# Optimization experiments

Hardware: AMD Instinct MI355X
Metric: run time of the kernel (lower is better)

The kernel has to match this reference:

```python
import jax, jax.numpy as jnp
import numpy as np

N_OPS = 15  # Bell(4) equivariant basis for square 2nd-order -> 2nd-order

def setup_inputs() -> dict:
    key = jax.random.key(0)
    n = 100_000          # entity instances
    m = 1_000_000        # random off-diagonal pairs (mirrored -> symmetric pattern)
    d_in, d_out = 32, 32
    rng = np.random.default_rng(0)
    r = rng.integers(0, n, size=m)
    c = rng.integers(0, n, size=m)
    # symmetric sparsity pattern + full diagonal; nnz = 2m + n
    rows = np.concatenate([r, c, np.arange(n)]).astype(np.int32)
    cols = np.concatenate([c, r, np.arange(n)]).astype(np.int32)
    # transpose intersection: entry k <-> its mirrored entry
    trans_perm = np.concatenate([np.arange(m, 2 * m), np.arange(m),
                                 np.arange(2 * m, 2 * m + n)]).astype(np.int32)
    k1, k2 = jax.random.split(key)
    values = jax.random.normal(k1, (rows.shape[0], d_in), dtype=jnp.float32)
    stdv = 0.1 / np.sqrt(d_in)
    weights = jax.random.uniform(k2, (N_OPS, d_in, d_out), minval=-stdv, maxval=stdv,
                                 dtype=jnp.float32)
    bias = jnp.zeros((N_OPS,), jnp.float32)
    return {"values": values, "weights": weights, "bias": bias,
            "rows": jnp.asarray(rows), "cols": jnp.asarray(cols),
            "trans_perm": jnp.asarray(trans_perm), "n_nodes": n}


def reference(values, weights, bias, rows, cols, trans_perm, n_nodes):
    # values: [nnz, d_in] features of sparse matrix entries at (rows, cols)
    is_diag = (rows == cols)[:, None].astype(values.dtype)            # [nnz, 1]
    sum_r = jax.ops.segment_sum(values, rows, num_segments=n_nodes)   # pool over cols -> [n, d_in]
    sum_c = jax.ops.segment_sum(values, cols, num_segments=n_nodes)   # pool over rows -> [n, d_in]
    diag = jax.ops.segment_sum(values * is_diag, rows, num_segments=n_nodes)  # gather_diag -> [n, d_in]
    sum_all = values.sum(0)        # pool over both indices -> [d_in]
    diag_sum = diag.sum(0)         # pooled diagonal -> [d_in]
    W = weights
    # ops 1-2: identity intersection, transpose intersection
    out = values @ W[0] + values[trans_perm] @ W[1]
    # ops 3-8: pooled/diag vectors broadcast along rows or cols
    out += (sum_r @ W[2])[rows] + (sum_r @ W[3])[cols]
    out += (sum_c @ W[4])[rows] + (sum_c @ W[5])[cols]
    out += (diag @ W[6])[rows] + (diag @ W[7])[cols]
    # ops 9-12, 14: embedded into the diagonal of the output pattern
    diag_part = (sum_r @ W[8])[rows] + (sum_c @ W[9])[rows] + (diag @ W[10])[rows] \
                + (diag_sum @ W[11]) + (sum_all @ W[13])
    out += is_diag * diag_part
    # ops 13, 15: global scalars broadcast to every nnz
    out += diag_sum @ W[12] + sum_all @ W[14]
    # per-op scalar bias added to the whole output (Y = Y + op + bias[i])
    out += bias.sum()
    return out
```

## Files before the change

### kernel.cpp

```cpp
#include <hip/hip_runtime.h>

#define N_NODES 100000
#define D 32
#define CAP 40


__global__ void k1a_fill(const int* __restrict__ rows,
                         const int* __restrict__ cols,
                         const int* __restrict__ tp,
                         const float* __restrict__ values,
                         int nnz,
                         int* __restrict__ cnt,
                         int* __restrict__ list,
                         float* __restrict__ sum_r,
                         float* __restrict__ sum_c,
                         float* __restrict__ diag) {
  int e = blockIdx.x * blockDim.x + threadIdx.x;
  if (e >= nnz) return;
  int r = rows[e];
  int pos = atomicAdd(&cnt[r], 1);
  if (pos < CAP) {
    list[(size_t)r * CAP + pos] = e;
  } else {
    int t = tp[e];
    int c = cols[e];
    for (int f = 0; f < D; f++) {
      float ve = values[(size_t)e * D + f];
      unsafeAtomicAdd(&sum_r[(size_t)r * D + f], ve);
      unsafeAtomicAdd(&sum_c[(size_t)r * D + f], values[(size_t)t * D + f]);
      if (c == r) unsafeAtomicAdd(&diag[(size_t)r * D + f], ve);
    }
  }
}

__global__ void k1b_gather(const float* __restrict__ values,
                           const int* __restrict__ cols,
                           const int* __restrict__ tp,
                           const int* __restrict__ cnt,
                           const int* __restrict__ list,
                           int n,
                           float* __restrict__ sum_r,
                           float* __restrict__ sum_c,
                           float* __restrict__ diag) {
  int tid = blockIdx.x * blockDim.x + threadIdx.x;
  int f = tid & 31;
  int i = tid >> 5;
  if (i >= n) return;
  int m = cnt[i];
  if (m > CAP) m = CAP;
  const int* lst = list + (size_t)i * CAP;
  float accR = 0.f, accC = 0.f, accD = 0.f;
  int e = (m > 0) ? lst[0] : 0;
  for (int k = 0; k < m; k++) {
    int en = (k + 1 < m) ? lst[k + 1] : 0;
    int t = tp[e];
    int c = cols[e];
    float ve = values[(size_t)e * D + f];
    float vt = values[(size_t)t * D + f];
    accR += ve;
    accC += vt;
    if (c == i) accD += ve;
    e = en;
  }
  size_t o = (size_t)i * D + f;
  sum_r[o] += accR;
  sum_c[o] += accC;
  diag[o] += accD;
}

__global__ void k1c_reduce(const float* __restrict__ sum_r,
                           const float* __restrict__ diag,
                           int n,
                           float* __restrict__ sum_all,
                           float* __restrict__ diag_sum) {
  __shared__ float sa[D], sd[D];
  int tid = blockIdx.x * blockDim.x + threadIdx.x;
  int f = threadIdx.x & 31;
  int slot = tid >> 5;
  int nslots = (gridDim.x * blockDim.x) >> 5;
  if (threadIdx.x < D) { sa[threadIdx.x] = 0.f; sd[threadIdx.x] = 0.f; }
  __syncthreads();
  float la = 0.f, ld = 0.f;
  for (int i = slot; i < n; i += nslots) {
    la += sum_r[(size_t)i * D + f];
    ld += diag[(size_t)i * D + f];
  }
  atomicAdd(&sa[f], la);
  atomicAdd(&sd[f], ld);
  __syncthreads();
  if (threadIdx.x < D) {
    unsafeAtomicAdd(&sum_all[threadIdx.x], sa[threadIdx.x]);
    unsafeAtomicAdd(&diag_sum[threadIdx.x], sd[threadIdx.x]);
  }
}

__global__ void k1_segsums(const float* __restrict__ values,
                           const int* __restrict__ rows,
                           const int* __restrict__ cols,
                           int nnz,
                           float* __restrict__ sum_r,
                           float* __restrict__ sum_c,
                           float* __restrict__ diag,
                           float* __restrict__ sum_all,
                           float* __restrict__ diag_sum) {
  int tid = blockIdx.x * blockDim.x + threadIdx.x;
  int f = tid & 31;
  int slot = tid >> 5;
  int nslots = (gridDim.x * blockDim.x) >> 5;
  float local_all = 0.f, local_diag = 0.f;
  for (int e = slot; e < nnz; e += nslots) {
    float v = values[(size_t)e * D + f];
    int r = rows[e];
    int c = cols[e];
    unsafeAtomicAdd(&sum_r[(size_t)r * D + f], v);
    unsafeAtomicAdd(&sum_c[(size_t)c * D + f], v);
    local_all += v;
    if (r == c) {
      unsafeAtomicAdd(&diag[(size_t)r * D + f], v);
      local_diag += v;
    }
  }
  unsafeAtomicAdd(&sum_all[f], local_all);
  unsafeAtomicAdd(&diag_sum[f], local_diag);
}

__global__ void k_globals(const float* __restrict__ W,
                          const float* __restrict__ bias,
                          const float* __restrict__ sum_all,
                          const float* __restrict__ diag_sum,
                          float* __restrict__ g,
                          float* __restrict__ gd) {
  int j = threadIdx.x;
  if (j >= D) return;
  float bt = 0.f;
  for (int i = 0; i < 15; i++) bt += bias[i];
  float a = bt, b = 0.f;
  for (int k = 0; k < D; k++) {
    float ds = diag_sum[k];
    float sa = sum_all[k];
    a = fmaf(ds, W[12 * 1024 + k * D + j], a);
    a = fmaf(sa, W[14 * 1024 + k * D + j], a);
    b = fmaf(ds, W[11 * 1024 + k * D + j], b);
    b = fmaf(sa, W[13 * 1024 + k * D + j], b);
  }
  g[j] = a;
  gd[j] = b;
}

__device__ __forceinline__ void triple_acc(float accA[D], float accB[D], float accD[D],
                                           const float* __restrict__ src,
                                           const float* __restrict__ wa,
                                           const float* __restrict__ wb,
                                           const float* __restrict__ wd) {
  const float4* s4 = (const float4*)src;
  for (int q = 0; q < 8; q++) {
    float4 t = s4[q];
    const float* wa_q = wa + q * 128;
    const float* wb_q = wb + q * 128;
    const float* wd_q = wd + q * 128;
#pragma unroll
    for (int j = 0; j < D; j++) {
      float a = accA[j], b = accB[j], d = accD[j];
      a = fmaf(t.x, wa_q[j], a);
      a = fmaf(t.y, wa_q[32 + j], a);
      a = fmaf(t.z, wa_q[64 + j], a);
      a = fmaf(t.w, wa_q[96 + j], a);
      b = fmaf(t.x, wb_q[j], b);
      b = fmaf(t.y, wb_q[32 + j], b);
      b = fmaf(t.z, wb_q[64 + j], b);
      b = fmaf(t.w, wb_q[96 + j], b);
      d = fmaf(t.x, wd_q[j], d);
      d = fmaf(t.y, wd_q[32 + j], d);
      d = fmaf(t.z, wd_q[64 + j], d);
      d = fmaf(t.w, wd_q[96 + j], d);
      accA[j] = a; accB[j] = b; accD[j] = d;
    }
  }
}

__global__ void k2_node_transform(const float* __restrict__ W, int n,
                                  float* __restrict__ sum_r,
                                  float* __restrict__ sum_c,
                                  float* __restrict__ diag) {
  int i = blockIdx.x * blockDim.x + threadIdx.x;
  if (i >= n) return;
  float accA[D], accB[D], accD[D];
#pragma unroll
  for (int j = 0; j < D; j++) { accA[j] = 0.f; accB[j] = 0.f; accD[j] = 0.f; }
  const float* sr = sum_r + (size_t)i * D;
  const float* sc = sum_c + (size_t)i * D;
  const float* dg = diag + (size_t)i * D;
  triple_acc(accA, accB, accD, sr, W + 2 * 1024, W + 3 * 1024, W + 8 * 1024);
  triple_acc(accA, accB, accD, sc, W + 4 * 1024, W + 5 * 1024, W + 9 * 1024);
  triple_acc(accA, accB, accD, dg, W + 6 * 1024, W + 7 * 1024, W + 10 * 1024);
  float4* oA = (float4*)(sum_r + (size_t)i * D);
  float4* oB = (float4*)(sum_c + (size_t)i * D);
  float4* oD = (float4*)(diag + (size_t)i * D);
#pragma unroll
  for (int q = 0; q < 8; q++) {
    oA[q] = make_float4(accA[4 * q], accA[4 * q + 1], accA[4 * q + 2], accA[4 * q + 3]);
    oB[q] = make_float4(accB[4 * q], accB[4 * q + 1], accB[4 * q + 2], accB[4 * q + 3]);
    oD[q] = make_float4(accD[4 * q], accD[4 * q + 1], accD[4 * q + 2], accD[4 * q + 3]);
  }
}

__device__ __forceinline__ void matvec_acc32(float acc[D],
                                             const float* __restrict__ src,
                                             const float* __restrict__ w) {
  const float4* s4 = (const float4*)src;
#pragma unroll 2
  for (int q = 0; q < 8; q++) {
    float4 t = s4[q];
    const float* wq = w + q * 128;
#pragma unroll
    for (int j = 0; j < D; j++) {
      float a = acc[j];
      a = fmaf(t.x, wq[j], a);
      a = fmaf(t.y, wq[32 + j], a);
      a = fmaf(t.z, wq[64 + j], a);
      a = fmaf(t.w, wq[96 + j], a);
      acc[j] = a;
    }
  }
}

__global__ void k3_out(const float* __restrict__ values,
                       const float* __restrict__ W,
                       const int* __restrict__ rows,
                       const int* __restrict__ cols,
                       const int* __restrict__ tp,
                       const float* __restrict__ A,
                       const float* __restrict__ B,
                       const float* __restrict__ Dg,
                       const float* __restrict__ g,
                       const float* __restrict__ gd,
                       int nnz,
                       float* __restrict__ out) {
  int e = blockIdx.x * blockDim.x + threadIdx.x;
  if (e >= nnz) return;
  int r = rows[e];
  int c = cols[e];
  int t = tp[e];
  float acc[D];
  const float4* Ar = (const float4*)(A + (size_t)r * D);
  const float4* Bc = (const float4*)(B + (size_t)c * D);
  const float4* G = (const float4*)g;
#pragma unroll
  for (int q = 0; q < 8; q++) {
    float4 a = Ar[q];
    float4 b = Bc[q];
    float4 gg = G[q];
    acc[4 * q + 0] = a.x + b.x + gg.x;
    acc[4 * q + 1] = a.y + b.y + gg.y;
    acc[4 * q + 2] = a.z + b.z + gg.z;
    acc[4 * q + 3] = a.w + b.w + gg.w;
  }
  if (r == c) {
    const float4* Dr = (const float4*)(Dg + (size_t)r * D);
    const float4* Gd = (const float4*)gd;
#pragma unroll
    for (int q = 0; q < 8; q++) {
      float4 d = Dr[q];
      float4 h = Gd[q];
      acc[4 * q + 0] += d.x + h.x;
      acc[4 * q + 1] += d.y + h.y;
      acc[4 * q + 2] += d.z + h.z;
      acc[4 * q + 3] += d.w + h.w;
    }
  }
  matvec_acc32(acc, values + (size_t)e * D, W);
  matvec_acc32(acc, values + (size_t)t * D, W + 1024);
  float4* o = (float4*)(out + (size_t)e * D);
#pragma unroll
  for (int q = 0; q < 8; q++) {
    o[q] = make_float4(acc[4 * q], acc[4 * q + 1], acc[4 * q + 2], acc[4 * q + 3]);
  }
}

extern "C" void kernel_launch(void* const* d_in, const int* in_sizes, int n_in,
                              void* d_out, int out_size, void* d_ws, size_t ws_size,
                              hipStream_t stream) {
  const float* values = (const float*)d_in[0];
  const float* W = (const float*)d_in[1];
  const float* bias = (const float*)d_in[2];
  const int* rows = (const int*)d_in[3];
  const int* cols = (const int*)d_in[4];
  const int* tp = (const int*)d_in[5];
  const int nnz = in_sizes[3];
  const int n = N_NODES;

  float* ws = (float*)d_ws;
  float* sum_r = ws;
  float* sum_c = sum_r + (size_t)n * D;
  float* diag = sum_c + (size_t)n * D;
  float* sum_all = diag + (size_t)n * D;
  float* diag_sum = sum_all + D;
  float* g = diag_sum + D;
  float* gd = g + D;
  int* cnt = (int*)(gd + D);
  int* list = cnt + n;

  const size_t base_floats = (size_t)3 * n * D + 4 * D;
  const size_t need = base_floats * sizeof(float)
                    + (size_t)n * sizeof(int)
                    + (size_t)n * CAP * sizeof(int);
  if (ws_size >= need) {
    hipMemsetAsync(ws, 0, base_floats * sizeof(float) + (size_t)n * sizeof(int),
                   stream);
    k1a_fill<<<(nnz + 255) / 256, 256, 0, stream>>>(rows, cols, tp, values, nnz,
                                                    cnt, list, sum_r, sum_c, diag);
    k1b_gather<<<((n * 32) + 255) / 256, 256, 0, stream>>>(values, cols, tp,
                                                           cnt, list, n,
                                                           sum_r, sum_c, diag);
    k1c_reduce<<<256, 256, 0, stream>>>(sum_r, diag, n, sum_all, diag_sum);
  } else {
    hipMemsetAsync(ws, 0, ((size_t)3 * n * D + 2 * D) * sizeof(float), stream);
    k1_segsums<<<2048, 256, 0, stream>>>(values, rows, cols, nnz,
                                         sum_r, sum_c, diag, sum_all, diag_sum);
  }
  k_globals<<<1, 64, 0, stream>>>(W, bias, sum_all, diag_sum, g, gd);
  k2_node_transform<<<(n + 255) / 256, 256, 0, stream>>>(W, n, sum_r, sum_c, diag);
  k3_out<<<(nnz + 255) / 256, 256, 0, stream>>>(values, W, rows, cols, tp,
                                                sum_r, sum_c, diag, g, gd,
                                                nnz, (float*)d_out);
}
```

Baseline: 1.248 ms.

## Pair mirrored entries in output kernel and fuse global reduction into gather

```diff
diff --git a/kernel.cpp b/kernel.cpp
--- a/kernel.cpp
+++ b/kernel.cpp
@@ -3,6 +3,8 @@
 #define N_NODES 100000
 #define D 32
 #define CAP 40
+
+typedef float f32x4 __attribute__((ext_vector_type(4)));
 
 
 __global__ void k1a_fill(const int* __restrict__ rows,
@@ -41,52 +43,64 @@
                            int n,
                            float* __restrict__ sum_r,
                            float* __restrict__ sum_c,
-                           float* __restrict__ diag) {
+                           float* __restrict__ diag,
+                           float* __restrict__ sum_all,
+                           float* __restrict__ diag_sum) {
+  __shared__ float sa[D], sd[D];
+  if (threadIdx.x < D) { sa[threadIdx.x] = 0.f; sd[threadIdx.x] = 0.f; }
+  __syncthreads();
+
   int tid = blockIdx.x * blockDim.x + threadIdx.x;
   int f = tid & 31;
   int i = tid >> 5;
-  if (i >= n) return;
-  int m = cnt[i];
-  if (m > CAP) m = CAP;
-  const int* lst = list + (size_t)i * CAP;
-  float accR = 0.f, accC = 0.f, accD = 0.f;
-  int e = (m > 0) ? lst[0] : 0;
-  for (int k = 0; k < m; k++) {
-    int en = (k + 1 < m) ? lst[k + 1] : 0;
-    int t = tp[e];
-    int c = cols[e];
-    float ve = values[(size_t)e * D + f];
-    float vt = values[(size_t)t * D + f];
-    accR += ve;
-    accC += vt;
-    if (c == i) accD += ve;
-    e = en;
-  }
-  size_t o = (size_t)i * D + f;
-  sum_r[o] += accR;
-  sum_c[o] += accC;
-  diag[o] += accD;
-}
-
-__global__ void k1c_reduce(const float* __restrict__ sum_r,
-                           const float* __restrict__ diag,
-                           int n,
-                           float* __restrict__ sum_all,
-                           float* __restrict__ diag_sum) {
-  __shared__ float sa[D], sd[D];
-  int tid = blockIdx.x * blockDim.x + threadIdx.x;
-  int f = threadIdx.x & 31;
-  int slot = tid >> 5;
-  int nslots = (gridDim.x * blockDim.x) >> 5;
-  if (threadIdx.x < D) { sa[threadIdx.x] = 0.f; sd[threadIdx.x] = 0.f; }
-  __syncthreads();
-  float la = 0.f, ld = 0.f;
-  for (int i = slot; i < n; i += nslots) {
-    la += sum_r[(size_t)i * D + f];
-    ld += diag[(size_t)i * D + f];
-  }
-  atomicAdd(&sa[f], la);
-  atomicAdd(&sd[f], ld);
+  float totR = 0.f, totD = 0.f;
+  if (i < n) {
+    int m = cnt[i];
+    if (m > CAP) m = CAP;
+    const int* lst = list + (size_t)i * CAP;
+    float accR = 0.f, accC = 0.f, accD = 0.f;
+    int k = 0;
+    for (; k + 4 <= m; k += 4) {
+      int4 e4 = *(const int4*)(lst + k);
+      int t0 = tp[e4.x], t1 = tp[e4.y], t2 = tp[e4.z], t3 = tp[e4.w];
+      int c0 = cols[e4.x], c1 = cols[e4.y], c2 = cols[e4.z], c3 = cols[e4.w];
+      float v0 = values[(size_t)e4.x * D + f];
+      float v1 = values[(size_t)e4.y * D + f];
+      float v2 = values[(size_t)e4.z * D + f];
+      float v3 = values[(size_t)e4.w * D + f];
+      float u0 = values[(size_t)t0 * D + f];
+      float u1 = values[(size_t)t1 * D + f];
+      float u2 = values[(size_t)t2 * D + f];
+      float u3 = values[(size_t)t3 * D + f];
+      accR += (v0 + v1) + (v2 + v3);
+      accC += (u0 + u1) + (u2 + u3);
+      if (c0 == i) accD += v0;
+      if (c1 == i) accD += v1;
+      if (c2 == i) accD += v2;
+      if (c3 == i) accD += v3;
+    }
+    for (; k < m; k++) {
+      int e = lst[k];
+      int t = tp[e];
+      int c = cols[e];
+      float ve = values[(size_t)e * D + f];
+      float vt = values[(size_t)t * D + f];
+      accR += ve;
+      accC += vt;
+      if (c == i) accD += ve;
+    }
+    size_t o = (size_t)i * D + f;
+    float pr = sum_r[o];
+    float pc = sum_c[o];
+    float pd = diag[o];
+    totR = pr + accR;
+    totD = pd + accD;
+    sum_r[o] = totR;
+    sum_c[o] = pc + accC;
+    diag[o] = totD;
+  }
+  atomicAdd(&sa[f], totR);
+  atomicAdd(&sd[f], totD);
   __syncthreads();
   if (threadIdx.x < D) {
     unsafeAtomicAdd(&sum_all[threadIdx.x], sa[threadIdx.x]);
@@ -204,23 +218,100 @@
   }
 }
 
-__device__ __forceinline__ void matvec_acc32(float acc[D],
-                                             const float* __restrict__ src,
-                                             const float* __restrict__ w) {
-  const float4* s4 = (const float4*)src;
+__device__ __forceinline__ void dual_acc(float accA[D], float accB[D],
+                                         const f32x4* __restrict__ s4,
+                                         const float* __restrict__ wa,
+                                         const float* __restrict__ wb) {
 #pragma unroll 2
   for (int q = 0; q < 8; q++) {
-    float4 t = s4[q];
-    const float* wq = w + q * 128;
+    f32x4 x = __builtin_nontemporal_load(s4 + q);
+    const float* wa_q = wa + q * 128;
+    const float* wb_q = wb + q * 128;
+#pragma unroll
+    for (int j = 0; j < D; j++) {
+      float a = accA[j], b = accB[j];
+      a = fmaf(x.x, wa_q[j], a);
+      a = fmaf(x.y, wa_q[32 + j], a);
+      a = fmaf(x.z, wa_q[64 + j], a);
+      a = fmaf(x.w, wa_q[96 + j], a);
+      b = fmaf(x.x, wb_q[j], b);
+      b = fmaf(x.y, wb_q[32 + j], b);
+      b = fmaf(x.z, wb_q[64 + j], b);
+      b = fmaf(x.w, wb_q[96 + j], b);
+      accA[j] = a; accB[j] = b;
+    }
+  }
+}
+
+__device__ __forceinline__ void both_acc(float acc[D],
+                                         const f32x4* __restrict__ s4,
+                                         const float* __restrict__ w0,
+                                         const float* __restrict__ w1) {
+#pragma unroll 2
+  for (int q = 0; q < 8; q++) {
+    f32x4 x = __builtin_nontemporal_load(s4 + q);
+    const float* w0q = w0 + q * 128;
+    const float* w1q = w1 + q * 128;
 #pragma unroll
     for (int j = 0; j < D; j++) {
       float a = acc[j];
-      a = fmaf(t.x, wq[j], a);
-      a = fmaf(t.y, wq[32 + j], a);
-      a = fmaf(t.z, wq[64 + j], a);
-      a = fmaf(t.w, wq[96 + j], a);
+      a = fmaf(x.x, w0q[j], a);
+      a = fmaf(x.y, w0q[32 + j], a);
+      a = fmaf(x.z, w0q[64 + j], a);
+      a = fmaf(x.w, w0q[96 + j], a);
+      a = fmaf(x.x, w1q[j], a);
+      a = fmaf(x.y, w1q[32 + j], a);
+      a = fmaf(x.z, w1q[64 + j], a);
+      a = fmaf(x.w, w1q[96 + j], a);
       acc[j] = a;
     }
+  }
+}
+
+__device__ __forceinline__ void base_acc(float acc[D], const float* __restrict__ A,
+                                         const float* __restrict__ B,
+                                         const float* __restrict__ Dg,
+                                         const float* __restrict__ g,
+                                         const float* __restrict__ gd,
+                                         int r, int c) {
+  const float4* Ar = (const float4*)(A + (size_t)r * D);
+  const float4* Bc = (const float4*)(B + (size_t)c * D);
+  const float4* G = (const float4*)g;
+#pragma unroll
+  for (int q = 0; q < 8; q++) {
+    float4 a = Ar[q];
+    float4 b = Bc[q];
+    float4 gg = G[q];
+    acc[4 * q + 0] = a.x + b.x + gg.x;
+    acc[4 * q + 1] = a.y + b.y + gg.y;
+    acc[4 * q + 2] = a.z + b.z + gg.z;
+    acc[4 * q + 3] = a.w + b.w + gg.w;
+  }
+  if (r == c) {
+    const float4* Dr = (const float4*)(Dg + (size_t)r * D);
+    const float4* Gd = (const float4*)gd;
+#pragma unroll
+    for (int q = 0; q < 8; q++) {
+      float4 d = Dr[q];
+      float4 h = Gd[q];
+      acc[4 * q + 0] += d.x + h.x;
+      acc[4 * q + 1] += d.y + h.y;
+      acc[4 * q + 2] += d.z + h.z;
+      acc[4 * q + 3] += d.w + h.w;
+    }
+  }
+}
+
+__device__ __forceinline__ void nt_store32(float* __restrict__ dst, const float acc[D]) {
+  f32x4* o = (f32x4*)dst;
+#pragma unroll
+  for (int q = 0; q < 8; q++) {
+    f32x4 v;
+    v.x = acc[4 * q];
+    v.y = acc[4 * q + 1];
+    v.z = acc[4 * q + 2];
+    v.w = acc[4 * q + 3];
+    __builtin_nontemporal_store(v, o + q);
   }
 }
 
@@ -238,42 +329,24 @@
                        float* __restrict__ out) {
   int e = blockIdx.x * blockDim.x + threadIdx.x;
   if (e >= nnz) return;
-  int r = rows[e];
-  int c = cols[e];
   int t = tp[e];
-  float acc[D];
-  const float4* Ar = (const float4*)(A + (size_t)r * D);
-  const float4* Bc = (const float4*)(B + (size_t)c * D);
-  const float4* G = (const float4*)g;
-#pragma unroll
-  for (int q = 0; q < 8; q++) {
-    float4 a = Ar[q];
-    float4 b = Bc[q];
-    float4 gg = G[q];
-    acc[4 * q + 0] = a.x + b.x + gg.x;
-    acc[4 * q + 1] = a.y + b.y + gg.y;
-    acc[4 * q + 2] = a.z + b.z + gg.z;
-    acc[4 * q + 3] = a.w + b.w + gg.w;
-  }
-  if (r == c) {
-    const float4* Dr = (const float4*)(Dg + (size_t)r * D);
-    const float4* Gd = (const float4*)gd;
-#pragma unroll
-    for (int q = 0; q < 8; q++) {
-      float4 d = Dr[q];
-      float4 h = Gd[q];
-      acc[4 * q + 0] += d.x + h.x;
-      acc[4 * q + 1] += d.y + h.y;
-      acc[4 * q + 2] += d.z + h.z;
-      acc[4 * q + 3] += d.w + h.w;
-    }
-  }
-  matvec_acc32(acc, values + (size_t)e * D, W);
-  matvec_acc32(acc, values + (size_t)t * D, W + 1024);
-  float4* o = (float4*)(out + (size_t)e * D);
-#pragma unroll
-  for (int q = 0; q < 8; q++) {
-    o[q] = make_float4(acc[4 * q], acc[4 * q + 1], acc[4 * q + 2], acc[4 * q + 3]);
+  if (t < e) return;
+  int re = rows[e], ce = cols[e];
+  const f32x4* ve = (const f32x4*)(values + (size_t)e * D);
+  float accE[D];
+  base_acc(accE, A, B, Dg, g, gd, re, ce);
+  if (t == e) {
+    both_acc(accE, ve, W, W + 1024);
+    nt_store32(out + (size_t)e * D, accE);
+  } else {
+    int rt = rows[t], ct = cols[t];
+    const f32x4* vt = (const f32x4*)(values + (size_t)t * D);
+    float accT[D];
+    base_acc(accT, A, B, Dg, g, gd, rt, ct);
+    dual_acc(accE, accT, ve, W, W + 1024);
+    dual_acc(accT, accE, vt, W, W + 1024);
+    nt_store32(out + (size_t)e * D, accE);
+    nt_store32(out + (size_t)t * D, accT);
   }
 }
 
@@ -305,16 +378,14 @@
                     + (size_t)n * sizeof(int)
                     + (size_t)n * CAP * sizeof(int);
   if (ws_size >= need) {
-    hipMemsetAsync(ws, 0, base_floats * sizeof(float) + (size_t)n * sizeof(int),
-                   stream);
+    (void)hipMemsetAsync(ws, 0, base_floats * sizeof(float) + (size_t)n * sizeof(int),
+                         stream);
     k1a_fill<<<(nnz + 255) / 256, 256, 0, stream>>>(rows, cols, tp, values, nnz,
                                                     cnt, list, sum_r, sum_c, diag);
-    k1b_gather<<<((n * 32) + 255) / 256, 256, 0, stream>>>(values, cols, tp,
-                                                           cnt, list, n,
-                                                           sum_r, sum_c, diag);
-    k1c_reduce<<<256, 256, 0, stream>>>(sum_r, diag, n, sum_all, diag_sum);
+    k1b_gather<<<(int)(((size_t)n * 32 + 255) / 256), 256, 0, stream>>>(
+        values, cols, tp, cnt, list, n, sum_r, sum_c, diag, sum_all, diag_sum);
   } else {
-    hipMemsetAsync(ws, 0, ((size_t)3 * n * D + 2 * D) * sizeof(float), stream);
+    (void)hipMemsetAsync(ws, 0, ((size_t)3 * n * D + 2 * D) * sizeof(float), stream);
     k1_segsums<<<2048, 256, 0, stream>>>(values, rows, cols, nnz,
                                          sum_r, sum_c, diag, sum_all, diag_sum);
   }
```

New measurement: 1.545 ms. 23.7% more time.
